# Kernel tuning notes

Hardware: AMD Instinct MI355X
Metric: run time of the kernel (lower is better)

Reference implementation:

```python
import jax, jax.numpy as jnp
import numpy as np

NUM_HEAD = 12
DIM_MODEL = 768
HEAD_DIM = DIM_MODEL // NUM_HEAD


def setup_inputs() -> dict:
    key = jax.random.key(0)
    ks = jax.random.split(key, 4)
    B, S, D = 2, 2048, DIM_MODEL
    scale = 1.0 / np.sqrt(D)
    return {
        "v1": jax.random.normal(ks[0], (B, S, D), dtype=jnp.float32),
        "v1_mask": jnp.zeros((B, 1, 1, S), dtype=jnp.float32),
        "Wq": jax.random.normal(ks[1], (D, D), dtype=jnp.float32) * scale,
        "bq": jnp.zeros((D,), dtype=jnp.float32),
        "Wk": jax.random.normal(ks[2], (D, D), dtype=jnp.float32) * scale,
        "bk": jnp.zeros((D,), dtype=jnp.float32),
        "Wv": jax.random.normal(ks[3], (D, D), dtype=jnp.float32) * scale,
        "bv": jnp.zeros((D,), dtype=jnp.float32),
    }


def reference(v1, v1_mask, Wq, bq, Wk, bk, Wv, bv):
    B, S, D = v1.shape
    H, hd = NUM_HEAD, HEAD_DIM

    def split_heads(x):  # [B,S,D] -> [B,H,S,hd]
        return x.reshape(B, S, H, hd).transpose(0, 2, 1, 3)

    q = split_heads(v1 @ Wq + bq)
    k = split_heads(v1 @ Wk + bk)
    v = split_heads(v1 @ Wv + bv)

    scores = jnp.einsum("bhqd,bhkd->bhqk", q, k) / jnp.sqrt(jnp.float32(hd))
    scores = scores + v1_mask  # additive mask broadcasts over heads/query
    probs = jax.nn.softmax(scores, axis=-1)
    # dropout is identity in eval/reference mode
    ctx = jnp.einsum("bhqk,bhkd->bhqd", probs, v)
    return ctx.transpose(0, 2, 1, 3).reshape(B, S, D)
```

## Files before the change

### kernel.cpp

```cpp
#include <hip/hip_runtime.h>
#include <math.h>

#define B_SZ 2
#define S_SZ 2048
#define D_SZ 768
#define NH   12
#define HD   64
#define BH_T (B_SZ * NH)
#define M_TOT (B_SZ * S_SZ)

using bfrag = __attribute__((ext_vector_type(8))) short;
using ffrag = __attribute__((ext_vector_type(4))) float;

__device__ __forceinline__ unsigned short f2bf(float f) {
    unsigned int u = __float_as_uint(f);
    u += 0x7fffu + ((u >> 16) & 1u);
    return (unsigned short)(u >> 16);
}
__device__ __forceinline__ unsigned short f2bf_fast(float f) {
    return (unsigned short)((__float_as_uint(f) + 0x8000u) >> 16);
}

__device__ __forceinline__ void async16(void* lds, const void* gp) {
    __builtin_amdgcn_global_load_lds(
        (const __attribute__((address_space(1))) unsigned int*)gp,
        (__attribute__((address_space(3))) unsigned int*)lds,
        16, 0, 0);
}

__global__ __launch_bounds__(256) void prep(
    const float* __restrict__ v1,
    const float* __restrict__ Wq, const float* __restrict__ Wk,
    const float* __restrict__ Wv,
    unsigned short* __restrict__ v1b, unsigned short* __restrict__ Wt) {
    __shared__ float tile[64][65];
    const int bx = blockIdx.x;
    const int t = threadIdx.x;
    if (bx < 3072) {
        int i = (bx * 256 + t) * 4;
        float4 v = *(const float4*)&v1[i];
        ushort4 o;
        o.x = f2bf(v.x); o.y = f2bf(v.y); o.z = f2bf(v.z); o.w = f2bf(v.w);
        *(ushort4*)&v1b[i] = o;
    } else {
        int r = bx - 3072;
        int z = r / 144;
        int rr = r % 144;
        int n0 = (rr % 12) * 64, k0 = (rr / 12) * 64;
        const float* W = (z == 0) ? Wq : (z == 1) ? Wk : Wv;
        unsigned short* dst = Wt + (size_t)z * D_SZ * D_SZ;
        #pragma unroll
        for (int i = 0; i < 16; ++i) {
            int flat = i * 256 + t;
            int rr2 = flat >> 6, c = flat & 63;
            tile[rr2][c] = W[(size_t)(k0 + rr2) * D_SZ + n0 + c];
        }
        __syncthreads();
        #pragma unroll
        for (int i = 0; i < 16; ++i) {
            int flat = i * 256 + t;
            int rr2 = flat >> 6, c = flat & 63;
            dst[(size_t)(n0 + rr2) * D_SZ + k0 + c] = f2bf(tile[c][rr2]);
        }
    }
}

#define CP_LD 136
#define CPV_LD 72

__global__ __launch_bounds__(256) void proj_gemm(
    const unsigned short* __restrict__ Ab,
    const unsigned short* __restrict__ Wt,
    const float* __restrict__ bq, const float* __restrict__ bk_,
    const float* __restrict__ bv_,
    unsigned short* __restrict__ Qb, unsigned short* __restrict__ Kb,
    unsigned short* __restrict__ Vtb) {
    const int z = blockIdx.z;
    const unsigned short* Bt = Wt + (size_t)z * D_SZ * D_SZ;
    const float* bias = (z == 0) ? bq : (z == 1) ? bk_ : bv_;

    __shared__ unsigned short smem[2][64 * 64 + 128 * 64];
    const int t = threadIdx.x;
    const int lane = t & 63;
    const int w = t >> 6;
    const int wm = w & 1, wn = w >> 1;
    const int col = lane & 15;
    const int quad = lane >> 4;
    const int m0 = blockIdx.y * 64;
    const int n0 = blockIdx.x * 128;
    const int wbase = t & ~63;

    ffrag acc[2][4];
    #pragma unroll
    for (int i = 0; i < 2; ++i)
        #pragma unroll
        for (int j = 0; j < 4; ++j) { ffrag zf = {0.f, 0.f, 0.f, 0.f}; acc[i][j] = zf; }

    #pragma unroll
    for (int i = 0; i < 2; ++i) {
        int c = i * 256 + t;
        int row = c >> 3;
        int gcol = ((c & 7) ^ (row & 7)) * 8;
        async16(&smem[0][(size_t)(i * 256 + wbase) * 8],
                &Ab[(size_t)(m0 + row) * D_SZ + gcol]);
    }
    #pragma unroll
    for (int i = 0; i < 4; ++i) {
        int c = i * 256 + t;
        int row = c >> 3;
        int gcol = ((c & 7) ^ (row & 7)) * 8;
        async16(&smem[0][64 * 64 + (size_t)(i * 256 + wbase) * 8],
                &Bt[(size_t)(n0 + row) * D_SZ + gcol]);
    }

    const int nIter = D_SZ / 64;
    for (int it = 0; it < nIter; ++it) {
        const int cur = it & 1;
        __syncthreads();
        if (it + 1 < nIter) {
            const int kn = (it + 1) * 64;
            #pragma unroll
            for (int i = 0; i < 2; ++i) {
                int c = i * 256 + t;
                int row = c >> 3;
                int gcol = ((c & 7) ^ (row & 7)) * 8;
                async16(&smem[cur ^ 1][(size_t)(i * 256 + wbase) * 8],
                        &Ab[(size_t)(m0 + row) * D_SZ + kn + gcol]);
            }
            #pragma unroll
            for (int i = 0; i < 4; ++i) {
                int c = i * 256 + t;
                int row = c >> 3;
                int gcol = ((c & 7) ^ (row & 7)) * 8;
                async16(&smem[cur ^ 1][64 * 64 + (size_t)(i * 256 + wbase) * 8],
                        &Bt[(size_t)(n0 + row) * D_SZ + kn + gcol]);
            }
        }
        const unsigned short* As = &smem[cur][0];
        const unsigned short* Bs = &smem[cur][64 * 64];
        #pragma unroll
        for (int kk = 0; kk < 64; kk += 32) {
            const int cc = (kk >> 3) + quad;
            bfrag a[2], b[4];
            #pragma unroll
            for (int mi = 0; mi < 2; ++mi) {
                int row = wm * 32 + mi * 16 + col;
                a[mi] = *(const bfrag*)&As[row * 64 + ((cc ^ (row & 7)) * 8)];
            }
            #pragma unroll
            for (int ni = 0; ni < 4; ++ni) {
                int row = wn * 64 + ni * 16 + col;
                b[ni] = *(const bfrag*)&Bs[row * 64 + ((cc ^ (row & 7)) * 8)];
            }
            if (z == 2) {
                #pragma unroll
                for (int mi = 0; mi < 2; ++mi)
                    #pragma unroll
                    for (int ni = 0; ni < 4; ++ni)
                        acc[mi][ni] = __builtin_amdgcn_mfma_f32_16x16x32_bf16(
                            a[mi], b[ni], acc[mi][ni], 0, 0, 0);
            } else {
                #pragma unroll
                for (int mi = 0; mi < 2; ++mi)
                    #pragma unroll
                    for (int ni = 0; ni < 4; ++ni)
                        acc[mi][ni] = __builtin_amdgcn_mfma_f32_16x16x32_bf16(
                            b[ni], a[mi], acc[mi][ni], 0, 0, 0);
            }
        }
    }

    __syncthreads();
    unsigned short* rp = &smem[0][0];

    if (z < 2) {
        const float sc = (z == 0) ? 0.125f : 1.0f;
        #pragma unroll
        for (int mi = 0; mi < 2; ++mi) {
            int m_local = wm * 32 + mi * 16 + col;
            #pragma unroll
            for (int ni = 0; ni < 4; ++ni) {
                int n_base = wn * 64 + ni * 16 + quad * 4;
                float4 b4 = *(const float4*)&bias[n0 + n_base];
                uint2 pk;
                pk.x = (unsigned)f2bf((acc[mi][ni][0] + b4.x) * sc) |
                       ((unsigned)f2bf((acc[mi][ni][1] + b4.y) * sc) << 16);
                pk.y = (unsigned)f2bf((acc[mi][ni][2] + b4.z) * sc) |
                       ((unsigned)f2bf((acc[mi][ni][3] + b4.w) * sc) << 16);
                *(uint2*)&rp[m_local * CP_LD + n_base] = pk;
            }
        }
        __syncthreads();
        unsigned short* Out = (z == 0) ? Qb : Kb;
        #pragma unroll
        for (int j = 0; j < 4; ++j) {
            int flat = j * 256 + t;
            int row = flat >> 4;
            int ch = flat & 15;
            uint4 vv = *(const uint4*)&rp[row * CP_LD + ch * 8];
            int m = m0 + row;
            int bb = m >> 11, s = m & 2047;
            int h = (n0 >> 6) + (ch >> 3);
            int d = (ch & 7) * 8;
            *(uint4*)&Out[((size_t)(bb * NH + h) * S_SZ + s) * HD + d] = vv;
        }
    } else {
        #pragma unroll
        for (int ni = 0; ni < 4; ++ni) {
            int n_local = wn * 64 + ni * 16 + col;
            float bvv = bias[n0 + n_local];
            #pragma unroll
            for (int mi = 0; mi < 2; ++mi) {
                int m_base = wm * 32 + mi * 16 + quad * 4;
                uint2 pk;
                pk.x = (unsigned)f2bf(acc[mi][ni][0] + bvv) |
                       ((unsigned)f2bf(acc[mi][ni][1] + bvv) << 16);
                pk.y = (unsigned)f2bf(acc[mi][ni][2] + bvv) |
                       ((unsigned)f2bf(acc[mi][ni][3] + bvv) << 16);
                *(uint2*)&rp[n_local * CPV_LD + m_base] = pk;
            }
        }
        __syncthreads();
        #pragma unroll
        for (int j = 0; j < 4; ++j) {
            int flat = j * 256 + t;
            int row = flat >> 3;
            int ch = flat & 7;
            uint4 vv = *(const uint4*)&rp[row * CPV_LD + ch * 8];
            int n = n0 + row;
            int h = n >> 6, d = n & 63;
            int m = m0 + ch * 8;
            int bb = m >> 11, s = m & 2047;
            *(uint4*)&Vtb[((size_t)(bb * NH + h) * HD + d) * S_SZ + s] = vv;
        }
    }
}

__global__ __launch_bounds__(256) void attn_mfma(
    const unsigned short* __restrict__ Qb, const unsigned short* __restrict__ Kb,
    const unsigned short* __restrict__ Vt, const float* __restrict__ mask,
    float* __restrict__ out) {
    __shared__ unsigned short Ks[2][64 * 64];
    __shared__ unsigned short Vs[2][64 * 64];
    __shared__ unsigned short Ps[4][16 * 64];

    const int t = threadIdx.x;
    const int lane = t & 63;
    const int w = t >> 6;
    const int col = lane & 15;
    const int quad = lane >> 4;
    const int q0 = blockIdx.x * 64;
    const int bh = blockIdx.y;
    const int b = bh / NH, h = bh % NH;
    const int wbase = t & ~63;

    const unsigned short* Qg = Qb + (size_t)bh * S_SZ * HD;
    const unsigned short* Kg = Kb + (size_t)bh * S_SZ * HD;
    const unsigned short* Vg = Vt + (size_t)bh * S_SZ * HD;
    const float* mrow = mask + (size_t)b * S_SZ;

    const int arow = w * 16 + col;
    bfrag aq[2];
    #pragma unroll
    for (int kk = 0; kk < 2; ++kk)
        aq[kk] = *(const bfrag*)&Qg[(size_t)(q0 + arow) * HD + (kk * 4 + quad) * 8];

    int srw[2], sgc[2];
    #pragma unroll
    for (int i = 0; i < 2; ++i) {
        int c = i * 256 + t;
        srw[i] = c >> 3;
        sgc[i] = ((c & 7) ^ (srw[i] & 7)) * 8;
    }

    #pragma unroll
    for (int i = 0; i < 2; ++i) {
        async16(&Ks[0][(size_t)(i * 256 + wbase) * 8],
                &Kg[(size_t)srw[i] * HD + sgc[i]]);
        async16(&Vs[0][(size_t)(i * 256 + wbase) * 8],
                &Vg[(size_t)srw[i] * S_SZ + sgc[i]]);
    }
    float mcur[4], mnext[4];
    #pragma unroll
    for (int ni = 0; ni < 4; ++ni) mcur[ni] = mrow[ni * 16 + col];

    ffrag o[4];
    #pragma unroll
    for (int i = 0; i < 4; ++i) { ffrag zf = {0.f, 0.f, 0.f, 0.f}; o[i] = zf; }
    float lsum[4] = {0.f, 0.f, 0.f, 0.f};

    const int nIter = S_SZ / 64;
    for (int it = 0; it < nIter; ++it) {
        const int cur = it & 1;
        __syncthreads();
        if (it + 1 < nIter) {
            const int kn = (it + 1) * 64;
            #pragma unroll
            for (int i = 0; i < 2; ++i) {
                async16(&Ks[cur ^ 1][(size_t)(i * 256 + wbase) * 8],
                        &Kg[(size_t)(kn + srw[i]) * HD + sgc[i]]);
                async16(&Vs[cur ^ 1][(size_t)(i * 256 + wbase) * 8],
                        &Vg[(size_t)srw[i] * S_SZ + kn + sgc[i]]);
            }
            #pragma unroll
            for (int ni = 0; ni < 4; ++ni) mnext[ni] = mrow[kn + ni * 16 + col];
        }

        ffrag s[4];
        #pragma unroll
        for (int i = 0; i < 4; ++i) { ffrag zf = {0.f, 0.f, 0.f, 0.f}; s[i] = zf; }
        #pragma unroll
        for (int kk = 0; kk < 2; ++kk) {
            const int cc = kk * 4 + quad;
            #pragma unroll
            for (int ni = 0; ni < 4; ++ni) {
                int brow = ni * 16 + col;
                bfrag bk8 = *(const bfrag*)&Ks[cur][brow * 64 + ((cc ^ (brow & 7)) * 8)];
                s[ni] = __builtin_amdgcn_mfma_f32_16x16x32_bf16(aq[kk], bk8, s[ni], 0, 0, 0);
            }
        }

        #pragma unroll
        for (int ni = 0; ni < 4; ++ni) {
            #pragma unroll
            for (int r = 0; r < 4; ++r) {
                float e = __expf(s[ni][r] + mcur[ni]);
                s[ni][r] = e;
                lsum[r] += e;
            }
        }

        unsigned short* Pw = &Ps[w][0];
        #pragma unroll
        for (int ni = 0; ni < 4; ++ni) {
            #pragma unroll
            for (int r = 0; r < 4; ++r) {
                int prow = quad * 4 + r;
                int pcol = ni * 16 + col;
                Pw[prow * 64 + (((pcol >> 3) ^ (prow & 7)) * 8) + (pcol & 7)] =
                    f2bf_fast(s[ni][r]);
            }
        }
        #pragma unroll
        for (int kk = 0; kk < 2; ++kk) {
            const int cc = kk * 4 + quad;
            bfrag ap = *(const bfrag*)&Pw[col * 64 + ((cc ^ (col & 7)) * 8)];
            #pragma unroll
            for (int di = 0; di < 4; ++di) {
                int vrow = di * 16 + col;
                bfrag bv8 = *(const bfrag*)&Vs[cur][vrow * 64 + ((cc ^ (vrow & 7)) * 8)];
                o[di] = __builtin_amdgcn_mfma_f32_16x16x32_bf16(ap, bv8, o[di], 0, 0, 0);
            }
        }

        #pragma unroll
        for (int ni = 0; ni < 4; ++ni) mcur[ni] = mnext[ni];
    }

    #pragma unroll
    for (int r = 0; r < 4; ++r) {
        #pragma unroll
        for (int off = 1; off < 16; off <<= 1)
            lsum[r] += __shfl_xor(lsum[r], off);
    }
    float inv[4];
    #pragma unroll
    for (int r = 0; r < 4; ++r) inv[r] = 1.0f / lsum[r];
    #pragma unroll
    for (int di = 0; di < 4; ++di) {
        int d = di * 16 + col;
        #pragma unroll
        for (int r = 0; r < 4; ++r) {
            int q = q0 + w * 16 + quad * 4 + r;
            out[((size_t)(b * S_SZ + q)) * D_SZ + h * HD + d] = o[di][r] * inv[r];
        }
    }
}

extern "C" void kernel_launch(void* const* d_in, const int* in_sizes, int n_in,
                              void* d_out, int out_size, void* d_ws, size_t ws_size,
                              hipStream_t stream) {
    const float* v1   = (const float*)d_in[0];
    const float* mask = (const float*)d_in[1];
    const float* Wq   = (const float*)d_in[2];
    const float* bq   = (const float*)d_in[3];
    const float* Wk   = (const float*)d_in[4];
    const float* bk   = (const float*)d_in[5];
    const float* Wv   = (const float*)d_in[6];
    const float* bv   = (const float*)d_in[7];
    float* out = (float*)d_out;

    char* ws = (char*)d_ws;
    const size_t per_b = (size_t)BH_T * S_SZ * HD * 2;
    unsigned short* Qb  = (unsigned short*)(ws);
    unsigned short* Kb  = (unsigned short*)(ws + per_b);
    unsigned short* Vtb = (unsigned short*)(ws + 2 * per_b);
    unsigned short* v1b = (unsigned short*)(ws + 3 * per_b);
    unsigned short* Wt  = (unsigned short*)(ws + 3 * per_b + (size_t)M_TOT * D_SZ * 2);

    prep<<<dim3(3072 + 432), 256, 0, stream>>>(v1, Wq, Wk, Wv, v1b, Wt);
    proj_gemm<<<dim3(6, 64, 3), 256, 0, stream>>>(v1b, Wt, bq, bk, bv, Qb, Kb, Vtb);
    attn_mfma<<<dim3(32, 24), 256, 0, stream>>>(Qb, Kb, Vtb, mask, out);
}
```

Baseline: 158.5 us.

## Enlarge projection GEMM M-tile to 128 and use exp2 with folded log2e scale

The projection GEMM tile grows from 64x128 to 128x128, so each block does 4x4 MFMA fragments per wave and the grid halves. This increases reuse of the weight tile and cuts global loads per output. It also means more registers, more LDS, and fewer blocks (576) to spread across CUs. Separately, the Q scale now folds in log2(e), and the mask is multiplied by log2(e), so attention uses the native v_exp_f32 (exp2) in place of __expf.

```diff
diff --git a/kernel.cpp b/kernel.cpp
--- a/kernel.cpp
+++ b/kernel.cpp
@@ -19,6 +19,16 @@
 }
 __device__ __forceinline__ unsigned short f2bf_fast(float f) {
     return (unsigned short)((__float_as_uint(f) + 0x8000u) >> 16);
+}
+
+__device__ __forceinline__ float fexp2(float x) {
+#if __has_builtin(__builtin_amdgcn_exp2f)
+    return __builtin_amdgcn_exp2f(x);
+#else
+    float r;
+    asm("v_exp_f32 %0, %1" : "=v"(r) : "v"(x));
+    return r;
+#endif
 }
 
 __device__ __forceinline__ void async16(void* lds, const void* gp) {
@@ -65,8 +75,7 @@
     }
 }
 
-#define CP_LD 136
-#define CPV_LD 72
+#define RP_LD 136
 
 __global__ __launch_bounds__(256) void proj_gemm(
     const unsigned short* __restrict__ Ab,
@@ -79,25 +88,26 @@
     const unsigned short* Bt = Wt + (size_t)z * D_SZ * D_SZ;
     const float* bias = (z == 0) ? bq : (z == 1) ? bk_ : bv_;
 
-    __shared__ unsigned short smem[2][64 * 64 + 128 * 64];
+    __shared__ __attribute__((aligned(16)))
+        unsigned short smem[2][128 * 64 + 128 * 64];
     const int t = threadIdx.x;
     const int lane = t & 63;
     const int w = t >> 6;
     const int wm = w & 1, wn = w >> 1;
     const int col = lane & 15;
     const int quad = lane >> 4;
-    const int m0 = blockIdx.y * 64;
+    const int m0 = blockIdx.y * 128;
     const int n0 = blockIdx.x * 128;
     const int wbase = t & ~63;
 
-    ffrag acc[2][4];
-    #pragma unroll
-    for (int i = 0; i < 2; ++i)
+    ffrag acc[4][4];
+    #pragma unroll
+    for (int i = 0; i < 4; ++i)
         #pragma unroll
         for (int j = 0; j < 4; ++j) { ffrag zf = {0.f, 0.f, 0.f, 0.f}; acc[i][j] = zf; }
 
     #pragma unroll
-    for (int i = 0; i < 2; ++i) {
+    for (int i = 0; i < 4; ++i) {
         int c = i * 256 + t;
         int row = c >> 3;
         int gcol = ((c & 7) ^ (row & 7)) * 8;
@@ -109,7 +119,7 @@
         int c = i * 256 + t;
         int row = c >> 3;
         int gcol = ((c & 7) ^ (row & 7)) * 8;
-        async16(&smem[0][64 * 64 + (size_t)(i * 256 + wbase) * 8],
+        async16(&smem[0][128 * 64 + (size_t)(i * 256 + wbase) * 8],
                 &Bt[(size_t)(n0 + row) * D_SZ + gcol]);
     }
 
@@ -120,7 +130,7 @@
         if (it + 1 < nIter) {
             const int kn = (it + 1) * 64;
             #pragma unroll
-            for (int i = 0; i < 2; ++i) {
+            for (int i = 0; i < 4; ++i) {
                 int c = i * 256 + t;
                 int row = c >> 3;
                 int gcol = ((c & 7) ^ (row & 7)) * 8;
@@ -132,19 +142,19 @@
                 int c = i * 256 + t;
                 int row = c >> 3;
                 int gcol = ((c & 7) ^ (row & 7)) * 8;
-                async16(&smem[cur ^ 1][64 * 64 + (size_t)(i * 256 + wbase) * 8],
+                async16(&smem[cur ^ 1][128 * 64 + (size_t)(i * 256 + wbase) * 8],
                         &Bt[(size_t)(n0 + row) * D_SZ + kn + gcol]);
             }
         }
         const unsigned short* As = &smem[cur][0];
-        const unsigned short* Bs = &smem[cur][64 * 64];
+        const unsigned short* Bs = &smem[cur][128 * 64];
         #pragma unroll
         for (int kk = 0; kk < 64; kk += 32) {
             const int cc = (kk >> 3) + quad;
-            bfrag a[2], b[4];
-            #pragma unroll
-            for (int mi = 0; mi < 2; ++mi) {
-                int row = wm * 32 + mi * 16 + col;
+            bfrag a[4], b[4];
+            #pragma unroll
+            for (int mi = 0; mi < 4; ++mi) {
+                int row = wm * 64 + mi * 16 + col;
                 a[mi] = *(const bfrag*)&As[row * 64 + ((cc ^ (row & 7)) * 8)];
             }
             #pragma unroll
@@ -154,14 +164,14 @@
             }
             if (z == 2) {
                 #pragma unroll
-                for (int mi = 0; mi < 2; ++mi)
+                for (int mi = 0; mi < 4; ++mi)
                     #pragma unroll
                     for (int ni = 0; ni < 4; ++ni)
                         acc[mi][ni] = __builtin_amdgcn_mfma_f32_16x16x32_bf16(
                             a[mi], b[ni], acc[mi][ni], 0, 0, 0);
             } else {
                 #pragma unroll
-                for (int mi = 0; mi < 2; ++mi)
+                for (int mi = 0; mi < 4; ++mi)
                     #pragma unroll
                     for (int ni = 0; ni < 4; ++ni)
                         acc[mi][ni] = __builtin_amdgcn_mfma_f32_16x16x32_bf16(
@@ -174,10 +184,10 @@
     unsigned short* rp = &smem[0][0];
 
     if (z < 2) {
-        const float sc = (z == 0) ? 0.125f : 1.0f;
-        #pragma unroll
-        for (int mi = 0; mi < 2; ++mi) {
-            int m_local = wm * 32 + mi * 16 + col;
+        const float sc = (z == 0) ? 0.18033688f : 1.0f;
+        #pragma unroll
+        for (int mi = 0; mi < 4; ++mi) {
+            int m_local = wm * 64 + mi * 16 + col;
             #pragma unroll
             for (int ni = 0; ni < 4; ++ni) {
                 int n_base = wn * 64 + ni * 16 + quad * 4;
@@ -187,17 +197,17 @@
                        ((unsigned)f2bf((acc[mi][ni][1] + b4.y) * sc) << 16);
                 pk.y = (unsigned)f2bf((acc[mi][ni][2] + b4.z) * sc) |
                        ((unsigned)f2bf((acc[mi][ni][3] + b4.w) * sc) << 16);
-                *(uint2*)&rp[m_local * CP_LD + n_base] = pk;
+                *(uint2*)&rp[m_local * RP_LD + n_base] = pk;
             }
         }
         __syncthreads();
         unsigned short* Out = (z == 0) ? Qb : Kb;
         #pragma unroll
-        for (int j = 0; j < 4; ++j) {
+        for (int j = 0; j < 8; ++j) {
             int flat = j * 256 + t;
             int row = flat >> 4;
             int ch = flat & 15;
-            uint4 vv = *(const uint4*)&rp[row * CP_LD + ch * 8];
+            uint4 vv = *(const uint4*)&rp[row * RP_LD + ch * 8];
             int m = m0 + row;
             int bb = m >> 11, s = m & 2047;
             int h = (n0 >> 6) + (ch >> 3);
@@ -210,23 +220,23 @@
             int n_local = wn * 64 + ni * 16 + col;
             float bvv = bias[n0 + n_local];
             #pragma unroll
-            for (int mi = 0; mi < 2; ++mi) {
-                int m_base = wm * 32 + mi * 16 + quad * 4;
+            for (int mi = 0; mi < 4; ++mi) {
+                int m_base = wm * 64 + mi * 16 + quad * 4;
                 uint2 pk;
                 pk.x = (unsigned)f2bf(acc[mi][ni][0] + bvv) |
                        ((unsigned)f2bf(acc[mi][ni][1] + bvv) << 16);
                 pk.y = (unsigned)f2bf(acc[mi][ni][2] + bvv) |
                        ((unsigned)f2bf(acc[mi][ni][3] + bvv) << 16);
-                *(uint2*)&rp[n_local * CPV_LD + m_base] = pk;
+                *(uint2*)&rp[n_local * RP_LD + m_base] = pk;
             }
         }
         __syncthreads();
         #pragma unroll
-        for (int j = 0; j < 4; ++j) {
+        for (int j = 0; j < 8; ++j) {
             int flat = j * 256 + t;
-            int row = flat >> 3;
-            int ch = flat & 7;
-            uint4 vv = *(const uint4*)&rp[row * CPV_LD + ch * 8];
+            int row = flat >> 4;
+            int ch = flat & 15;
+            uint4 vv = *(const uint4*)&rp[row * RP_LD + ch * 8];
             int n = n0 + row;
             int h = n >> 6, d = n & 63;
             int m = m0 + ch * 8;
@@ -282,7 +292,7 @@
     }
     float mcur[4], mnext[4];
     #pragma unroll
-    for (int ni = 0; ni < 4; ++ni) mcur[ni] = mrow[ni * 16 + col];
+    for (int ni = 0; ni < 4; ++ni) mcur[ni] = mrow[ni * 16 + col] * 1.44269504f;
 
     ffrag o[4];
     #pragma unroll
@@ -303,7 +313,8 @@
                         &Vg[(size_t)srw[i] * S_SZ + kn + sgc[i]]);
             }
             #pragma unroll
-            for (int ni = 0; ni < 4; ++ni) mnext[ni] = mrow[kn + ni * 16 + col];
+            for (int ni = 0; ni < 4; ++ni)
+                mnext[ni] = mrow[kn + ni * 16 + col] * 1.44269504f;
         }
 
         ffrag s[4];
@@ -324,7 +335,7 @@
         for (int ni = 0; ni < 4; ++ni) {
             #pragma unroll
             for (int r = 0; r < 4; ++r) {
-                float e = __expf(s[ni][r] + mcur[ni]);
+                float e = fexp2(s[ni][r] + mcur[ni]);
                 s[ni][r] = e;
                 lsum[r] += e;
             }
@@ -399,6 +410,6 @@
     unsigned short* Wt  = (unsigned short*)(ws + 3 * per_b + (size_t)M_TOT * D_SZ * 2);
 
     prep<<<dim3(3072 + 432), 256, 0, stream>>>(v1, Wq, Wk, Wv, v1b, Wt);
-    proj_gemm<<<dim3(6, 64, 3), 256, 0, stream>>>(v1b, Wt, bq, bk, bv, Qb, Kb, Vtb);
+    proj_gemm<<<dim3(6, 32, 3), 256, 0, stream>>>(v1b, Wt, bq, bk, bv, Qb, Kb, Vtb);
     attn_mfma<<<dim3(32, 24), 256, 0, stream>>>(Qb, Kb, Vtb, mask, out);
 }
```

Measured after the change: 157.0 us. Within noise of the previous version (-1.0%).
